# Optimization experiments

Measured on AMD Instinct MI355X. Metric: run time of the kernel, lower is better.

## Reference

```python
import jax, jax.numpy as jnp
import numpy as np

B, S, IN_DIM = 8, 4096, 1024
N_SLOTS, SLOT_DIM, N_HEADS, CHUNK, TOP_K = 64, 256, 4, 16, 3
EPS_LN = 1e-5


def setup_inputs() -> dict:
    key = jax.random.key(0)
    ks = jax.random.split(key, 8)
    std = 0.02
    return {
        "x": jax.random.normal(ks[0], (B, S, IN_DIM), jnp.float32),
        "slot_memory": jax.random.normal(ks[1], (1, N_SLOTS, SLOT_DIM), jnp.float32) * std,
        "slot_keys": jax.random.normal(ks[2], (N_SLOTS, SLOT_DIM), jnp.float32) * std,
        "W_in": jax.random.normal(ks[3], (IN_DIM, SLOT_DIM), jnp.float32) / np.sqrt(IN_DIM).astype(np.float32),
        "W_write": jax.random.normal(ks[4], (SLOT_DIM, SLOT_DIM), jnp.float32) / np.sqrt(SLOT_DIM).astype(np.float32),
        "W_gate": jax.random.normal(ks[5], (2 * SLOT_DIM, 1), jnp.float32) / np.sqrt(2 * SLOT_DIM).astype(np.float32),
        "b_gate": jnp.zeros((1,), jnp.float32),
        "W_out": jax.random.normal(ks[6], (SLOT_DIM, IN_DIM), jnp.float32) / np.sqrt(SLOT_DIM).astype(np.float32),
        "ln_in_scale": jnp.ones((IN_DIM,), jnp.float32),
        "ln_in_bias": jnp.zeros((IN_DIM,), jnp.float32),
        "ln_s_scale": jnp.ones((SLOT_DIM,), jnp.float32),
        "ln_s_bias": jnp.zeros((SLOT_DIM,), jnp.float32),
    }


def _layer_norm(x, scale, bias):
    m = jnp.mean(x, axis=-1, keepdims=True)
    v = jnp.mean((x - m) ** 2, axis=-1, keepdims=True)
    return (x - m) * jax.lax.rsqrt(v + EPS_LN) * scale + bias


def _l2norm(x):
    n = jnp.sqrt(jnp.sum(x * x, axis=-1, keepdims=True))
    return x / jnp.maximum(n, 1e-12)  # matches F.normalize eps


def _forward(x, slot_memory, slot_keys, W_in, W_write, W_gate, b_gate, W_out,
             ln_in_scale, ln_in_bias, ln_s_scale, ln_s_bias):
    Bx, Sx, _ = x.shape
    hd = SLOT_DIM // N_HEADS
    slots0 = jnp.broadcast_to(slot_memory, (Bx, N_SLOTS, SLOT_DIM))

    # ---- batched read attention over slots ----
    q = _layer_norm(x, ln_in_scale, ln_in_bias) @ W_in          # (B,S,D)
    qh = q.reshape(Bx, Sx, N_HEADS, hd)
    kh = slots0.reshape(Bx, N_SLOTS, N_HEADS, hd)               # k == v == slots
    scores = jnp.einsum('bshd,bnhd->bhsn', qh, kh) * (hd ** -0.5)
    attn = jax.nn.softmax(scores, axis=-1)                      # (B,H,S,N)
    read = jnp.einsum('bhsn,bnhd->bshd', attn, kh).reshape(Bx, Sx, SLOT_DIM)

    # ---- sequential chunked top-k gather/scatter slot write ----
    key_norms = _l2norm(slot_keys)                              # (N,D)
    b_idx = jnp.arange(Bx)[:, None]

    def chunk_step(slots, chunk):                               # chunk: (B,C,D)
        summary = chunk.mean(axis=1)                            # (B,D)
        match = _l2norm(summary) @ key_norms.T                  # (B,N) cosine sim
        _, top_idx = jax.lax.top_k(match, TOP_K)                # (B,K)
        wv = summary @ W_write                                  # (B,D)
        sel = jnp.take_along_axis(slots, top_idx[:, :, None], axis=1)  # (B,K,D)
        gate = jax.nn.sigmoid(
            jnp.concatenate([sel.mean(axis=1), wv], axis=-1) @ W_gate + b_gate)  # (B,1)
        g = gate[:, None, :]
        new_vals = (1.0 - g) * sel + g * wv[:, None, :]         # (B,K,D)
        return slots.at[b_idx, top_idx].set(new_vals), None

    chunks = read.reshape(Bx, Sx // CHUNK, CHUNK, SLOT_DIM).transpose(1, 0, 2, 3)
    slots_f, _ = jax.lax.scan(chunk_step, slots0, chunks)
    new_slots = _layer_norm(slots_f, ln_s_scale, ln_s_bias)

    out = read @ W_out                                          # dropout is identity in eval
    return out, new_slots


def reference(x, slot_memory, slot_keys, W_in, W_write, W_gate, b_gate, W_out,
              ln_in_scale, ln_in_bias, ln_s_scale, ln_s_bias):
    return _forward(x, slot_memory, slot_keys, W_in, W_write, W_gate, b_gate, W_out,
                    ln_in_scale, ln_in_bias, ln_s_scale, ln_s_bias)
```

## Files before the change

### kernel.cpp

```cpp
#include <hip/hip_runtime.h>

typedef __attribute__((ext_vector_type(8))) short s8v;
typedef __attribute__((ext_vector_type(4))) float f4v;

#define PAD1 88
#define PADK 40

__device__ __forceinline__ unsigned short f2bf(float f) {
  unsigned u = __float_as_uint(f);
  u += 0x7fffu + ((u >> 16) & 1u);
  return (unsigned short)(u >> 16);
}
__device__ __forceinline__ float bf2f(unsigned short h) {
  return __uint_as_float(((unsigned)h) << 16);
}
__device__ __forceinline__ f4v vmax4(f4v a, f4v b) {
  f4v r; r[0]=fmaxf(a[0],b[0]); r[1]=fmaxf(a[1],b[1]); r[2]=fmaxf(a[2],b[2]); r[3]=fmaxf(a[3],b[3]); return r;
}
__device__ __forceinline__ f4v shflxor4(f4v v, int m) {
  f4v r; r[0]=__shfl_xor(v[0],m); r[1]=__shfl_xor(v[1],m); r[2]=__shfl_xor(v[2],m); r[3]=__shfl_xor(v[3],m); return r;
}
__device__ __forceinline__ f4v exp4(f4v v) {
  f4v r; r[0]=__expf(v[0]); r[1]=__expf(v[1]); r[2]=__expf(v[2]); r[3]=__expf(v[3]); return r;
}

__global__ void k_prep(const float* __restrict__ W_in, const float* __restrict__ lnis,
                       const float* __restrict__ lnib, const float* __restrict__ W_out,
                       const float* __restrict__ skeys, const float* __restrict__ smem0,
                       const float* __restrict__ wgate,
                       unsigned short* __restrict__ wth, unsigned short* __restrict__ wtl,
                       unsigned short* __restrict__ wot, float* __restrict__ keyn,
                       float* __restrict__ d0, float* __restrict__ uvec, float* __restrict__ vvec)
{
  __shared__ float pr[4];
  const int bid = blockIdx.x, tid = threadIdx.x;
  if (bid < 1024) {
    int idx = bid * 256 + tid;
    int n = idx >> 10, k = idx & 1023;
    float val = lnis[k] * W_in[k * 256 + n];
    unsigned short h = f2bf(val);
    wth[idx] = h;
    wtl[idx] = f2bf(val - bf2f(h));
  } else if (bid < 2048) {
    int idx = (bid - 1024) * 256 + tid;
    int n = idx >> 8, k = idx & 255;
    wot[idx] = f2bf(W_out[k * 1024 + n]);
  } else if (bid == 2048) {
    float su = 0.f, sv = 0.f;
    for (int i = 0; i < 1024; ++i) {
      float wv_ = W_in[i * 256 + tid];
      su += lnis[i] * wv_;
      sv += lnib[i] * wv_;
    }
    uvec[tid] = su; vvec[tid] = sv;
  } else {
    int n = bid - 2049;
    float sk = skeys[n * 256 + tid];
    float sq = sk * sk;
    #pragma unroll
    for (int m = 32; m; m >>= 1) sq += __shfl_xor(sq, m);
    if ((tid & 63) == 0) pr[tid >> 6] = sq;
    __syncthreads();
    float tot = pr[0] + pr[1] + pr[2] + pr[3];
    keyn[n * 256 + tid] = sk * (1.0f / fmaxf(sqrtf(tot), 1e-12f));
    float pd = smem0[n * 256 + tid] * wgate[tid];
    #pragma unroll
    for (int m = 32; m; m >>= 1) pd += __shfl_xor(pd, m);
    __syncthreads();
    if ((tid & 63) == 0) pr[tid >> 6] = pd;
    __syncthreads();
    if (tid == 0) d0[n] = pr[0] + pr[1] + pr[2] + pr[3];
  }
}

__global__ __launch_bounds__(512, 2) void k_gemm1(const float* __restrict__ x,
    const unsigned short* __restrict__ wth, const unsigned short* __restrict__ wtl,
    const float* __restrict__ uvec, const float* __restrict__ vvec,
    float* __restrict__ q)
{
  __shared__ unsigned short Ah[128 * PADK], Al[128 * PADK];
  __shared__ unsigned short Bh[256 * PADK], Bl[256 * PADK];
  __shared__ float uls[256], vls[256];
  __shared__ float mls[128], rls[128];
  const int tid = threadIdx.x;
  const int w = tid >> 6, lane = tid & 63;
  const int wm = w >> 2, wn = w & 3;
  const int row0 = blockIdx.x * 128;
  if (tid < 256) { uls[tid] = uvec[tid]; vls[tid] = vvec[tid]; }
  f4v zz = {0.f, 0.f, 0.f, 0.f};
  f4v acc[4][4];
  #pragma unroll
  for (int i = 0; i < 4; ++i)
    #pragma unroll
    for (int j = 0; j < 4; ++j) acc[i][j] = zz;
  const int rowA = tid >> 2, kqA = (tid & 3) * 8;
  const int colB = tid >> 1, khB = (tid & 1) * 16;
  float ps = 0.f, pss = 0.f;
  for (int kt = 0; kt < 32; ++kt) {
    const int k0 = kt * 32;
    {
      const float* src = x + (size_t)(row0 + rowA) * 1024 + k0 + kqA;
      float vv[8];
      *(f4v*)vv = *(const f4v*)src;
      *(f4v*)(vv + 4) = *(const f4v*)(src + 4);
      unsigned short hh[8], ll[8];
      #pragma unroll
      for (int i = 0; i < 8; ++i) {
        ps += vv[i]; pss += vv[i] * vv[i];
        unsigned short hsh = f2bf(vv[i]);
        hh[i] = hsh;
        ll[i] = f2bf(vv[i] - bf2f(hsh));
      }
      *(s8v*)&Ah[rowA * PADK + kqA] = *(const s8v*)hh;
      *(s8v*)&Al[rowA * PADK + kqA] = *(const s8v*)ll;
      const unsigned short* sh = wth + (size_t)colB * 1024 + k0 + khB;
      const unsigned short* sl = wtl + (size_t)colB * 1024 + k0 + khB;
      *(s8v*)&Bh[colB * PADK + khB] = *(const s8v*)sh;
      *(s8v*)&Bh[colB * PADK + khB + 8] = *(const s8v*)(sh + 8);
      *(s8v*)&Bl[colB * PADK + khB] = *(const s8v*)sl;
      *(s8v*)&Bl[colB * PADK + khB + 8] = *(const s8v*)(sl + 8);
    }
    __syncthreads();
    {
      const int kb = (lane >> 4) * 8;
      s8v ah[4], al[4], bh[4], bl[4];
      #pragma unroll
      for (int mi = 0; mi < 4; ++mi) {
        const int rr = (wm * 64 + mi * 16 + (lane & 15)) * PADK + kb;
        ah[mi] = *(const s8v*)&Ah[rr];
        al[mi] = *(const s8v*)&Al[rr];
      }
      #pragma unroll
      for (int ni = 0; ni < 4; ++ni) {
        const int ccv = (wn * 64 + ni * 16 + (lane & 15)) * PADK + kb;
        bh[ni] = *(const s8v*)&Bh[ccv];
        bl[ni] = *(const s8v*)&Bl[ccv];
      }
      #pragma unroll
      for (int mi = 0; mi < 4; ++mi)
        #pragma unroll
        for (int ni = 0; ni < 4; ++ni) {
          acc[mi][ni] = __builtin_amdgcn_mfma_f32_16x16x32_bf16(ah[mi], bh[ni], acc[mi][ni], 0, 0, 0);
          acc[mi][ni] = __builtin_amdgcn_mfma_f32_16x16x32_bf16(ah[mi], bl[ni], acc[mi][ni], 0, 0, 0);
          acc[mi][ni] = __builtin_amdgcn_mfma_f32_16x16x32_bf16(al[mi], bh[ni], acc[mi][ni], 0, 0, 0);
        }
    }
    __syncthreads();
  }
  {
    float s0 = ps, s1 = pss;
    s0 += __shfl_xor(s0, 1); s1 += __shfl_xor(s1, 1);
    s0 += __shfl_xor(s0, 2); s1 += __shfl_xor(s1, 2);
    if ((tid & 3) == 0) {
      float mean = s0 * (1.0f / 1024.0f);
      mls[rowA] = mean;
      rls[rowA] = rsqrtf(s1 * (1.0f / 1024.0f) - mean * mean + 1e-5f);
    }
  }
  __syncthreads();
  #pragma unroll
  for (int mi = 0; mi < 4; ++mi)
    #pragma unroll
    for (int j = 0; j < 4; ++j) {
      const int lr = wm * 64 + mi * 16 + (lane >> 4) * 4 + j;
      const int r = row0 + lr;
      const float mv = mls[lr], rv = rls[lr];
      #pragma unroll
      for (int ni = 0; ni < 4; ++ni) {
        const int cidx = wn * 64 + ni * 16 + (lane & 15);
        q[(size_t)r * 256 + cidx] = rv * acc[mi][ni][j] - rv * mv * uls[cidx] + vls[cidx];
      }
    }
}

__global__ __launch_bounds__(512, 2) void k_attn(const float* __restrict__ q,
    const float* __restrict__ smem0, unsigned short* __restrict__ readb,
    float* __restrict__ summ)
{
  __shared__ float Kf[64 * 256];
  __shared__ float Pl[8][16 * 68];
  __shared__ float csm[8][64];
  const int tid = threadIdx.x;
  const int w = tid >> 6, lane = tid & 63;
  const int h = w & 3;
  const int l15 = lane & 15, kq = lane >> 4;

  {
    const int base = tid * 32;
    #pragma unroll
    for (int i = 0; i < 8; ++i)
      *(f4v*)&Kf[base + i * 4] = *(const f4v*)&smem0[base + i * 4];
  }
  __syncthreads();

  s8v bsh[4][2], bsl[4][2], bpv[4][2];
  #pragma unroll
  for (int nt = 0; nt < 4; ++nt)
    #pragma unroll
    for (int ks = 0; ks < 2; ++ks) {
      const float* src = &Kf[(nt * 16 + l15) * 256 + h * 64 + ks * 32 + kq * 8];
      float tmp[8];
      *(f4v*)tmp = *(const f4v*)src; *(f4v*)(tmp + 4) = *(const f4v*)(src + 4);
      unsigned short hh[8], ll[8];
      #pragma unroll
      for (int j = 0; j < 8; ++j) {
        hh[j] = f2bf(tmp[j]);
        ll[j] = f2bf(tmp[j] - bf2f(hh[j]));
      }
      bsh[nt][ks] = *(const s8v*)hh;
      bsl[nt][ks] = *(const s8v*)ll;
      unsigned short pp[8];
      #pragma unroll
      for (int j = 0; j < 8; ++j)
        pp[j] = f2bf(Kf[(ks * 32 + kq * 8 + j) * 256 + h * 64 + nt * 16 + l15]);
      bpv[nt][ks] = *(const s8v*)pp;
    }

  const int g0 = blockIdx.x * 8 + (w >> 2) * 4;
  f4v qv[2][4];
  {
    #pragma unroll
    for (int ks = 0; ks < 2; ++ks) {
      const float* qp = q + (size_t)(g0 * 16 + l15) * 256 + h * 64 + ks * 32 + kq * 8;
      qv[0][ks * 2] = *(const f4v*)qp;
      qv[0][ks * 2 + 1] = *(const f4v*)(qp + 4);
    }
  }
  #pragma unroll
  for (int i = 0; i < 4; ++i) {
    const int cur = i & 1, nxt = cur ^ 1;
    if (i < 3) {
      const int gn = g0 + i + 1;
      #pragma unroll
      for (int ks = 0; ks < 2; ++ks) {
        const float* qp = q + (size_t)(gn * 16 + l15) * 256 + h * 64 + ks * 32 + kq * 8;
        qv[nxt][ks * 2] = *(const f4v*)qp;
        qv[nxt][ks * 2 + 1] = *(const f4v*)(qp + 4);
      }
    }
    const int g = g0 + i;
    s8v ah[2], al[2];
    #pragma unroll
    for (int ks = 0; ks < 2; ++ks) {
      float tmp[8];
      *(f4v*)tmp = qv[cur][ks * 2]; *(f4v*)(tmp + 4) = qv[cur][ks * 2 + 1];
      unsigned short hh[8], ll[8];
      #pragma unroll
      for (int j = 0; j < 8; ++j) {
        hh[j] = f2bf(tmp[j]);
        ll[j] = f2bf(tmp[j] - bf2f(hh[j]));
      }
      ah[ks] = *(const s8v*)hh; al[ks] = *(const s8v*)ll;
    }
    f4v zz = {0.f, 0.f, 0.f, 0.f};
    f4v sacc[4] = {zz, zz, zz, zz};
    #pragma unroll
    for (int ks = 0; ks < 2; ++ks)
      #pragma unroll
      for (int nt = 0; nt < 4; ++nt) {
        sacc[nt] = __builtin_amdgcn_mfma_f32_16x16x32_bf16(ah[ks], bsh[nt][ks], sacc[nt], 0, 0, 0);
        sacc[nt] = __builtin_amdgcn_mfma_f32_16x16x32_bf16(ah[ks], bsl[nt][ks], sacc[nt], 0, 0, 0);
        sacc[nt] = __builtin_amdgcn_mfma_f32_16x16x32_bf16(al[ks], bsh[nt][ks], sacc[nt], 0, 0, 0);
      }
    #pragma unroll
    for (int nt = 0; nt < 4; ++nt) sacc[nt] = sacc[nt] * 0.125f;
    f4v mx = vmax4(vmax4(sacc[0], sacc[1]), vmax4(sacc[2], sacc[3]));
    #pragma unroll
    for (int m = 1; m <= 8; m <<= 1) mx = vmax4(mx, shflxor4(mx, m));
    f4v p[4];
    f4v psum = zz;
    #pragma unroll
    for (int nt = 0; nt < 4; ++nt) { p[nt] = exp4(sacc[nt] - mx); psum = psum + p[nt]; }
    #pragma unroll
    for (int m = 1; m <= 8; m <<= 1) psum = psum + shflxor4(psum, m);
    f4v rs;
    rs[0] = 1.0f / psum[0]; rs[1] = 1.0f / psum[1];
    rs[2] = 1.0f / psum[2]; rs[3] = 1.0f / psum[3];
    #pragma unroll
    for (int nt = 0; nt < 4; ++nt) p[nt] = p[nt] * rs;
    float cs4[4];
    #pragma unroll
    for (int nt = 0; nt < 4; ++nt) {
      cs4[nt] = p[nt][0] + p[nt][1] + p[nt][2] + p[nt][3];
      cs4[nt] += __shfl_xor(cs4[nt], 16);
      cs4[nt] += __shfl_xor(cs4[nt], 32);
    }
    if (kq == 0) {
      #pragma unroll
      for (int nt = 0; nt < 4; ++nt) csm[w][nt * 16 + l15] = cs4[nt];
    }
    #pragma unroll
    for (int nt = 0; nt < 4; ++nt)
      #pragma unroll
      for (int j = 0; j < 4; ++j)
        Pl[w][(kq * 4 + j) * 68 + nt * 16 + l15] = p[nt][j];
    s8v pa[2];
    #pragma unroll
    for (int ks = 0; ks < 2; ++ks) {
      const float* pp = &Pl[w][l15 * 68 + ks * 32 + kq * 8];
      float tmp[8];
      *(f4v*)tmp = *(const f4v*)pp; *(f4v*)(tmp + 4) = *(const f4v*)(pp + 4);
      unsigned short uu[8];
      #pragma unroll
      for (int j = 0; j < 8; ++j) uu[j] = f2bf(tmp[j]);
      pa[ks] = *(const s8v*)uu;
    }
    f4v racc[4] = {zz, zz, zz, zz};
    #pragma unroll
    for (int ks = 0; ks < 2; ++ks)
      #pragma unroll
      for (int nt = 0; nt < 4; ++nt)
        racc[nt] = __builtin_amdgcn_mfma_f32_16x16x32_bf16(pa[ks], bpv[nt][ks], racc[nt], 0, 0, 0);
    const int rowbase = (g >> 8) * 4096 + (g & 255) * 16;
    #pragma unroll
    for (int nt = 0; nt < 4; ++nt)
      #pragma unroll
      for (int j = 0; j < 4; ++j)
        readb[(size_t)(rowbase + kq * 4 + j) * 256 + h * 64 + nt * 16 + l15] = f2bf(racc[nt][j]);
    float s = 0.f;
    #pragma unroll 8
    for (int n = 0; n < 64; ++n) s += csm[w][n] * Kf[n * 256 + h * 64 + lane];
    summ[(size_t)g * 256 + h * 64 + lane] = s * (1.0f / 16.0f);
  }
}

__global__ void k_match(const float* __restrict__ summ, const float* __restrict__ keyn,
                        const float* __restrict__ Wwr, const float* __restrict__ wgate,
                        int* __restrict__ top3, float* __restrict__ wv,
                        float* __restrict__ wg2, float* __restrict__ dwv)
{
  __shared__ float sm[4][256];
  __shared__ float nrm_inv[4];
  __shared__ float mtch[4][64];
  __shared__ float redA[4][4], redB[4][4];
  const int tid = threadIdx.x, lane = tid & 63, w = tid >> 6;
  const int gbase = blockIdx.x * 4;
  #pragma unroll
  for (int gi = 0; gi < 4; ++gi) sm[gi][tid] = summ[(size_t)(gbase + gi) * 256 + tid];
  __syncthreads();
  {
    float ss = 0.f;
    #pragma unroll
    for (int i = 0; i < 4; ++i) { float vv_ = sm[w][lane + i * 64]; ss += vv_ * vv_; }
    #pragma unroll
    for (int m = 32; m; m >>= 1) ss += __shfl_xor(ss, m);
    if (lane == 0) nrm_inv[w] = 1.0f / fmaxf(sqrtf(ss), 1e-12f);
  }
  __syncthreads();
  {
    const int n = tid >> 2, qq = tid & 3;
    float mac[4] = {0.f, 0.f, 0.f, 0.f};
    const float* kp = keyn + n * 256 + qq * 64;
    for (int d = 0; d < 64; ++d) {
      float kv = kp[d];
      int dd = qq * 64 + d;
      mac[0] += sm[0][dd] * kv; mac[1] += sm[1][dd] * kv;
      mac[2] += sm[2][dd] * kv; mac[3] += sm[3][dd] * kv;
    }
    #pragma unroll
    for (int gi = 0; gi < 4; ++gi) {
      float v2_ = mac[gi];
      v2_ += __shfl_xor(v2_, 1);
      v2_ += __shfl_xor(v2_, 2);
      if (qq == 0) mtch[gi][n] = v2_ * nrm_inv[gi];
    }
  }
  __syncthreads();
  {
    float vorig = mtch[w][lane];
    #pragma unroll
    for (int it = 0; it < 3; ++it) {
      float rv = vorig; int ri = lane;
      #pragma unroll
      for (int m = 32; m; m >>= 1) {
        float ov = __shfl_xor(rv, m); int oi = __shfl_xor(ri, m);
        if (ov > rv || (ov == rv && oi < ri)) { rv = ov; ri = oi; }
      }
      if (lane == 0) top3[(gbase + w) * 4 + it] = ri;
      if (lane == ri) vorig = -3.0e38f;
    }
  }
  float wva[4] = {0.f, 0.f, 0.f, 0.f};
  for (int d = 0; d < 256; ++d) {
    float ww = Wwr[(size_t)d * 256 + tid];
    wva[0] += sm[0][d] * ww; wva[1] += sm[1][d] * ww;
    wva[2] += sm[2][d] * ww; wva[3] += sm[3][d] * ww;
  }
  const float g1 = wgate[tid], g2 = wgate[256 + tid];
  #pragma unroll
  for (int gi = 0; gi < 4; ++gi) {
    wv[(size_t)(gbase + gi) * 256 + tid] = wva[gi];
    float p2 = wva[gi] * g2, p1 = wva[gi] * g1;
    #pragma unroll
    for (int m = 32; m; m >>= 1) { p2 += __shfl_xor(p2, m); p1 += __shfl_xor(p1, m); }
    if (lane == 0) { redA[gi][w] = p2; redB[gi][w] = p1; }
  }
  __syncthreads();
  if (tid < 4) {
    wg2[gbase + tid] = redA[tid][0] + redA[tid][1] + redA[tid][2] + redA[tid][3];
    dwv[gbase + tid] = redB[tid][0] + redB[tid][1] + redB[tid][2] + redB[tid][3];
  }
}

__global__ __launch_bounds__(1024) void k_scan(const float* __restrict__ d0,
    const int* __restrict__ top3, const float* __restrict__ wg2, const float* __restrict__ dwv,
    const float* __restrict__ bgate, const float* __restrict__ wv,
    const float* __restrict__ smem0, const float* __restrict__ lnss,
    const float* __restrict__ lnsb, float* __restrict__ outns)
{
  __shared__ float Wl[256][64];
  __shared__ float pn[64];
  __shared__ float wvs[32][256];
  __shared__ float gls[256];
  __shared__ int   pprm[256][4];
  __shared__ float dsl[64];
  const int bb = blockIdx.x, tid = threadIdx.x;
  const int lane = tid & 63;

  int ixA[4], iyA[4], izA[4];
  if (tid < 64) {
    const float bg = bgate[0];
    const float L2E = 1.4426950408889634f;
    #pragma unroll
    for (int j = 0; j < 4; ++j) {
      const int c = j * 64 + tid;
      int4 t3 = *(const int4*)&top3[(bb * 256 + c) * 4];
      ixA[j] = t3.x; iyA[j] = t3.y; izA[j] = t3.z;
      pprm[c][0] = t3.x | (t3.y << 6) | (t3.z << 12);
      pprm[c][1] = __float_as_int(-(wg2[bb * 256 + c] + bg) * L2E);
      pprm[c][2] = __float_as_int(dwv[bb * 256 + c]);
      pprm[c][3] = 0;
    }
    dsl[tid] = d0[tid];
  }
  __syncthreads();

  if (tid == 0) {
    const float COEFN = -0.48089834696298783f;
    #pragma unroll 2
    for (int c = 0; c < 256; ++c) {
      const int4 pr = *(const int4*)&pprm[c][0];
      const int i0 = pr.x & 63, i1 = (pr.x >> 6) & 63, i2 = (pr.x >> 12) & 63;
      const float wz = __int_as_float(pr.y);
      const float dv = __int_as_float(pr.z);
      const float a = dsl[i0], b = dsl[i1], d2 = dsl[i2];
      const float s3 = a + b + d2;
      const float e = __builtin_amdgcn_exp2f(fmaf(s3, COEFN, wz));
      const float g = __builtin_amdgcn_rcpf(1.0f + e);
      gls[c] = g;
      dsl[i0] = fmaf(g, dv - a, a);
      dsl[i1] = fmaf(g, dv - b, b);
      dsl[i2] = fmaf(g, dv - d2, d2);
    }
  }
  __syncthreads();

  if (tid < 64) {
    float running = 1.0f;
    #pragma unroll
    for (int j = 3; j >= 0; --j) {
      #pragma unroll 1
      for (int sl = 63; sl >= 0; --sl) {
        const int a0 = __builtin_amdgcn_readlane(ixA[j], sl);
        const int a1 = __builtin_amdgcn_readlane(iyA[j], sl);
        const int a2 = __builtin_amdgcn_readlane(izA[j], sl);
        const float gv = gls[j * 64 + sl];
        const bool hit = (lane == a0) | (lane == a1) | (lane == a2);
        Wl[j * 64 + sl][lane] = hit ? gv * running : 0.f;
        running = hit ? running * (1.0f - gv) : running;
      }
    }
    pn[lane] = running;
  }
  __syncthreads();

  const int n = tid >> 4, dq = tid & 15;
  float acc[16];
  {
    const float p = pn[n];
    const float* v0p = smem0 + n * 256 + dq * 16;
    #pragma unroll
    for (int i = 0; i < 16; i += 4) {
      f4v v0 = *(const f4v*)(v0p + i);
      acc[i] = p * v0[0]; acc[i + 1] = p * v0[1];
      acc[i + 2] = p * v0[2]; acc[i + 3] = p * v0[3];
    }
  }
  const int rr = tid >> 5, cc8 = (tid & 31) * 8;
  for (int ct = 0; ct < 8; ++ct) {
    __syncthreads();
    {
      const float* src = wv + (size_t)(bb * 256 + ct * 32 + rr) * 256 + cc8;
      *(f4v*)&wvs[rr][cc8] = *(const f4v*)src;
      *(f4v*)&wvs[rr][cc8 + 4] = *(const f4v*)(src + 4);
    }
    __syncthreads();
    #pragma unroll 1
    for (int cc = 0; cc < 32; ++cc) {
      const float coef = Wl[ct * 32 + cc][n];
      if (coef != 0.f) {
        const float* wp = &wvs[cc][dq * 16];
        #pragma unroll
        for (int i4 = 0; i4 < 4; ++i4) {
          f4v wq = *(const f4v*)(wp + i4 * 4);
          acc[i4 * 4 + 0] += coef * wq[0];
          acc[i4 * 4 + 1] += coef * wq[1];
          acc[i4 * 4 + 2] += coef * wq[2];
          acc[i4 * 4 + 3] += coef * wq[3];
        }
      }
    }
  }

  float s1 = 0.f;
  #pragma unroll
  for (int i = 0; i < 16; ++i) s1 += acc[i];
  #pragma unroll
  for (int m = 1; m < 16; m <<= 1) s1 += __shfl_xor(s1, m);
  const float mean = s1 * (1.0f / 256.0f);
  float s2 = 0.f;
  #pragma unroll
  for (int i = 0; i < 16; ++i) { float dd = acc[i] - mean; s2 += dd * dd; }
  #pragma unroll
  for (int m = 1; m < 16; m <<= 1) s2 += __shfl_xor(s2, m);
  const float rstd = rsqrtf(s2 * (1.0f / 256.0f) + 1e-5f);
  {
    const int base = (bb * 64 + n) * 256 + dq * 16;
    #pragma unroll
    for (int i = 0; i < 16; ++i) {
      int dd = dq * 16 + i;
      outns[base + i] = (acc[i] - mean) * rstd * lnss[dd] + lnsb[dd];
    }
  }
}

__global__ __launch_bounds__(512, 2) void k_gemm2(const unsigned short* __restrict__ a,
    const unsigned short* __restrict__ wot, float* __restrict__ out)
{
  __shared__ unsigned short As[128 * PAD1];
  __shared__ unsigned short Bs[256 * PAD1];
  const int tid = threadIdx.x;
  const int w = tid >> 6, lane = tid & 63;
  const int wm = w >> 2, wn = w & 3;
  const int mblk = blockIdx.x >> 2, nblk = blockIdx.x & 3;
  const int row0 = mblk * 128, n0 = nblk * 256;
  f4v zz = {0.f, 0.f, 0.f, 0.f};
  f4v acc[4][4];
  #pragma unroll
  for (int i = 0; i < 4; ++i)
    #pragma unroll
    for (int j = 0; j < 4; ++j) acc[i][j] = zz;
  const int rowA = tid >> 2, kqA = (tid & 3) * 16;
  const int colB = tid >> 1, khB = (tid & 1) * 32;
  for (int kt = 0; kt < 4; ++kt) {
    const int k0 = kt * 64;
    {
      const unsigned short* src = a + (size_t)(row0 + rowA) * 256 + k0 + kqA;
      *(s8v*)&As[rowA * PAD1 + kqA] = *(const s8v*)src;
      *(s8v*)&As[rowA * PAD1 + kqA + 8] = *(const s8v*)(src + 8);
      const unsigned short* sb = wot + (size_t)(n0 + colB) * 256 + k0 + khB;
      unsigned short* db = &Bs[colB * PAD1 + khB];
      #pragma unroll
      for (int i = 0; i < 4; ++i) *(s8v*)(db + 8 * i) = *(const s8v*)(sb + 8 * i);
    }
    __syncthreads();
    #pragma unroll
    for (int kk = 0; kk < 64; kk += 32) {
      const int kb = kk + (lane >> 4) * 8;
      s8v af[4], bf[4];
      #pragma unroll
      for (int mi = 0; mi < 4; ++mi)
        af[mi] = *(const s8v*)&As[(wm * 64 + mi * 16 + (lane & 15)) * PAD1 + kb];
      #pragma unroll
      for (int ni = 0; ni < 4; ++ni)
        bf[ni] = *(const s8v*)&Bs[(wn * 64 + ni * 16 + (lane & 15)) * PAD1 + kb];
      #pragma unroll
      for (int mi = 0; mi < 4; ++mi)
        #pragma unroll
        for (int ni = 0; ni < 4; ++ni)
          acc[mi][ni] = __builtin_amdgcn_mfma_f32_16x16x32_bf16(af[mi], bf[ni], acc[mi][ni], 0, 0, 0);
    }
    __syncthreads();
  }
  #pragma unroll
  for (int mi = 0; mi < 4; ++mi)
    #pragma unroll
    for (int j = 0; j < 4; ++j) {
      const int r = row0 + wm * 64 + mi * 16 + (lane >> 4) * 4 + j;
      #pragma unroll
      for (int ni = 0; ni < 4; ++ni) {
        const int cidx = wn * 64 + ni * 16 + (lane & 15);
        out[(size_t)r * 1024 + n0 + cidx] = acc[mi][ni][j];
      }
    }
}

extern "C" void kernel_launch(void* const* d_in, const int* in_sizes, int n_in,
                              void* d_out, int out_size, void* d_ws, size_t ws_size,
                              hipStream_t stream) {
  const float* x      = (const float*)d_in[0];
  const float* smem   = (const float*)d_in[1];
  const float* skeys  = (const float*)d_in[2];
  const float* W_in   = (const float*)d_in[3];
  const float* W_wr   = (const float*)d_in[4];
  const float* wgate  = (const float*)d_in[5];
  const float* bgate  = (const float*)d_in[6];
  const float* W_out  = (const float*)d_in[7];
  const float* lnis   = (const float*)d_in[8];
  const float* lnib   = (const float*)d_in[9];
  const float* lnss   = (const float*)d_in[10];
  const float* lnsb   = (const float*)d_in[11];
  (void)in_sizes; (void)n_in; (void)out_size; (void)ws_size;

  char* ws = (char*)d_ws;
  float*          q_buf = (float*)(ws + 0);
  unsigned short* readb = (unsigned short*)(ws + 134217728);
  float*          summ  = (float*)(ws + 150994944);
  float*          wv    = (float*)(ws + 153092096);
  unsigned short* wth   = (unsigned short*)(ws + 155189248);
  unsigned short* wtl   = (unsigned short*)(ws + 155713536);
  unsigned short* wot   = (unsigned short*)(ws + 156237824);
  float*          keyn  = (float*)(ws + 156762112);
  float*          uvec  = (float*)(ws + 157089792);
  float*          vvec  = (float*)(ws + 157090816);
  float*          d0    = (float*)(ws + 157091840);
  int*            top3  = (int*)(ws + 157092096);
  float*          wg2   = (float*)(ws + 157124864);
  float*          dwv   = (float*)(ws + 157133056);

  float* out   = (float*)d_out;
  float* outns = out + 33554432;

  k_prep<<<dim3(2113), dim3(256), 0, stream>>>(W_in, lnis, lnib, W_out, skeys, smem, wgate,
                                               wth, wtl, wot, keyn, d0, uvec, vvec);
  k_gemm1<<<dim3(256), dim3(512), 0, stream>>>(x, wth, wtl, uvec, vvec, q_buf);
  k_attn<<<dim3(256), dim3(512), 0, stream>>>(q_buf, smem, readb, summ);
  k_match<<<dim3(512), dim3(256), 0, stream>>>(summ, keyn, W_wr, wgate, top3, wv, wg2, dwv);
  k_scan<<<dim3(8), dim3(1024), 0, stream>>>(d0, top3, wg2, dwv, bgate, wv, smem, lnss, lnsb, outns);
  k_gemm2<<<dim3(1024), dim3(512), 0, stream>>>(readb, wot, out);
}
```

Measured before the change: 354.4 us.

## Split gemm1 into 128x128 N-tiles with K=64 steps and higher occupancy

The input-projection GEMM now tiles its 256 output columns across two blocks (128x128 per block) instead of one 128x256 block, doubling the grid to 512 blocks. The K step per shared-memory stage grows from 32 to 64, with two MFMA sub-steps per barrier, and launch bounds ask for 4 blocks per CU. The aim is more parallelism and fewer barriers per K. The cost is that each x row block is loaded and split into bf16 hi/lo twice, once per N-half. The LayerNorm statistics are also recomputed in both blocks.

```diff
diff --git a/kernel.cpp b/kernel.cpp
--- a/kernel.cpp
+++ b/kernel.cpp
@@ -4,7 +4,7 @@
 typedef __attribute__((ext_vector_type(4))) float f4v;
 
 #define PAD1 88
-#define PADK 40
+#define PADG 72
 
 __device__ __forceinline__ unsigned short f2bf(float f) {
   unsigned u = __float_as_uint(f);
@@ -73,73 +73,76 @@
   }
 }
 
-__global__ __launch_bounds__(512, 2) void k_gemm1(const float* __restrict__ x,
+__global__ __launch_bounds__(512, 4) void k_gemm1(const float* __restrict__ x,
     const unsigned short* __restrict__ wth, const unsigned short* __restrict__ wtl,
     const float* __restrict__ uvec, const float* __restrict__ vvec,
     float* __restrict__ q)
 {
-  __shared__ unsigned short Ah[128 * PADK], Al[128 * PADK];
-  __shared__ unsigned short Bh[256 * PADK], Bl[256 * PADK];
-  __shared__ float uls[256], vls[256];
+  __shared__ unsigned short Ah[128 * PADG], Al[128 * PADG];
+  __shared__ unsigned short Bh[128 * PADG], Bl[128 * PADG];
+  __shared__ float uls[128], vls[128];
   __shared__ float mls[128], rls[128];
   const int tid = threadIdx.x;
   const int w = tid >> 6, lane = tid & 63;
   const int wm = w >> 2, wn = w & 3;
-  const int row0 = blockIdx.x * 128;
-  if (tid < 256) { uls[tid] = uvec[tid]; vls[tid] = vvec[tid]; }
+  const int mblk = blockIdx.x >> 1, nblk = blockIdx.x & 1;
+  const int row0 = mblk * 128, n0 = nblk * 128;
+  if (tid < 128) { uls[tid] = uvec[n0 + tid]; vls[tid] = vvec[n0 + tid]; }
   f4v zz = {0.f, 0.f, 0.f, 0.f};
-  f4v acc[4][4];
+  f4v acc[4][2];
   #pragma unroll
   for (int i = 0; i < 4; ++i)
     #pragma unroll
-    for (int j = 0; j < 4; ++j) acc[i][j] = zz;
-  const int rowA = tid >> 2, kqA = (tid & 3) * 8;
-  const int colB = tid >> 1, khB = (tid & 1) * 16;
+    for (int j = 0; j < 2; ++j) acc[i][j] = zz;
+  const int rowA = tid >> 2, kqA = (tid & 3) * 16;
   float ps = 0.f, pss = 0.f;
-  for (int kt = 0; kt < 32; ++kt) {
-    const int k0 = kt * 32;
+  for (int kt = 0; kt < 16; ++kt) {
+    const int k0 = kt * 64;
     {
       const float* src = x + (size_t)(row0 + rowA) * 1024 + k0 + kqA;
-      float vv[8];
-      *(f4v*)vv = *(const f4v*)src;
-      *(f4v*)(vv + 4) = *(const f4v*)(src + 4);
-      unsigned short hh[8], ll[8];
-      #pragma unroll
-      for (int i = 0; i < 8; ++i) {
+      float vv[16];
+      #pragma unroll
+      for (int i = 0; i < 4; ++i) *(f4v*)(vv + 4 * i) = *(const f4v*)(src + 4 * i);
+      unsigned short hh[16], ll[16];
+      #pragma unroll
+      for (int i = 0; i < 16; ++i) {
         ps += vv[i]; pss += vv[i] * vv[i];
         unsigned short hsh = f2bf(vv[i]);
         hh[i] = hsh;
         ll[i] = f2bf(vv[i] - bf2f(hsh));
       }
-      *(s8v*)&Ah[rowA * PADK + kqA] = *(const s8v*)hh;
-      *(s8v*)&Al[rowA * PADK + kqA] = *(const s8v*)ll;
-      const unsigned short* sh = wth + (size_t)colB * 1024 + k0 + khB;
-      const unsigned short* sl = wtl + (size_t)colB * 1024 + k0 + khB;
-      *(s8v*)&Bh[colB * PADK + khB] = *(const s8v*)sh;
-      *(s8v*)&Bh[colB * PADK + khB + 8] = *(const s8v*)(sh + 8);
-      *(s8v*)&Bl[colB * PADK + khB] = *(const s8v*)sl;
-      *(s8v*)&Bl[colB * PADK + khB + 8] = *(const s8v*)(sl + 8);
-    }
-    __syncthreads();
-    {
-      const int kb = (lane >> 4) * 8;
-      s8v ah[4], al[4], bh[4], bl[4];
+      *(s8v*)&Ah[rowA * PADG + kqA] = *(const s8v*)hh;
+      *(s8v*)&Ah[rowA * PADG + kqA + 8] = *(const s8v*)(hh + 8);
+      *(s8v*)&Al[rowA * PADG + kqA] = *(const s8v*)ll;
+      *(s8v*)&Al[rowA * PADG + kqA + 8] = *(const s8v*)(ll + 8);
+      const unsigned short* sh = wth + (size_t)(n0 + rowA) * 1024 + k0 + kqA;
+      const unsigned short* sl = wtl + (size_t)(n0 + rowA) * 1024 + k0 + kqA;
+      *(s8v*)&Bh[rowA * PADG + kqA] = *(const s8v*)sh;
+      *(s8v*)&Bh[rowA * PADG + kqA + 8] = *(const s8v*)(sh + 8);
+      *(s8v*)&Bl[rowA * PADG + kqA] = *(const s8v*)sl;
+      *(s8v*)&Bl[rowA * PADG + kqA + 8] = *(const s8v*)(sl + 8);
+    }
+    __syncthreads();
+    #pragma unroll
+    for (int kk = 0; kk < 64; kk += 32) {
+      const int kb = kk + (lane >> 4) * 8;
+      s8v ah[4], al[4], bh[2], bl[2];
       #pragma unroll
       for (int mi = 0; mi < 4; ++mi) {
-        const int rr = (wm * 64 + mi * 16 + (lane & 15)) * PADK + kb;
+        const int rr = (wm * 64 + mi * 16 + (lane & 15)) * PADG + kb;
         ah[mi] = *(const s8v*)&Ah[rr];
         al[mi] = *(const s8v*)&Al[rr];
       }
       #pragma unroll
-      for (int ni = 0; ni < 4; ++ni) {
-        const int ccv = (wn * 64 + ni * 16 + (lane & 15)) * PADK + kb;
+      for (int ni = 0; ni < 2; ++ni) {
+        const int ccv = (wn * 32 + ni * 16 + (lane & 15)) * PADG + kb;
         bh[ni] = *(const s8v*)&Bh[ccv];
         bl[ni] = *(const s8v*)&Bl[ccv];
       }
       #pragma unroll
       for (int mi = 0; mi < 4; ++mi)
         #pragma unroll
-        for (int ni = 0; ni < 4; ++ni) {
+        for (int ni = 0; ni < 2; ++ni) {
           acc[mi][ni] = __builtin_amdgcn_mfma_f32_16x16x32_bf16(ah[mi], bh[ni], acc[mi][ni], 0, 0, 0);
           acc[mi][ni] = __builtin_amdgcn_mfma_f32_16x16x32_bf16(ah[mi], bl[ni], acc[mi][ni], 0, 0, 0);
           acc[mi][ni] = __builtin_amdgcn_mfma_f32_16x16x32_bf16(al[mi], bh[ni], acc[mi][ni], 0, 0, 0);
@@ -166,9 +169,9 @@
       const int r = row0 + lr;
       const float mv = mls[lr], rv = rls[lr];
       #pragma unroll
-      for (int ni = 0; ni < 4; ++ni) {
-        const int cidx = wn * 64 + ni * 16 + (lane & 15);
-        q[(size_t)r * 256 + cidx] = rv * acc[mi][ni][j] - rv * mv * uls[cidx] + vls[cidx];
+      for (int ni = 0; ni < 2; ++ni) {
+        const int lc = wn * 32 + ni * 16 + (lane & 15);
+        q[(size_t)r * 256 + n0 + lc] = rv * acc[mi][ni][j] - rv * mv * uls[lc] + vls[lc];
       }
     }
 }
@@ -633,7 +636,7 @@
 
   k_prep<<<dim3(2113), dim3(256), 0, stream>>>(W_in, lnis, lnib, W_out, skeys, smem, wgate,
                                                wth, wtl, wot, keyn, d0, uvec, vvec);
-  k_gemm1<<<dim3(256), dim3(512), 0, stream>>>(x, wth, wtl, uvec, vvec, q_buf);
+  k_gemm1<<<dim3(512), dim3(512), 0, stream>>>(x, wth, wtl, uvec, vvec, q_buf);
   k_attn<<<dim3(256), dim3(512), 0, stream>>>(q_buf, smem, readb, summ);
   k_match<<<dim3(512), dim3(256), 0, stream>>>(summ, keyn, W_wr, wgate, top3, wv, wg2, dwv);
   k_scan<<<dim3(8), dim3(1024), 0, stream>>>(d0, top3, wg2, dwv, bgate, wv, smem, lnss, lnsb, outns);
```

Measured after the change: 337.9 us. 4.6% less time.
